# Kernel tuning notes

Measured on AMD Instinct MI355X. Metric: run time of the kernel, lower is better.

The kernel has to match this reference:

```python
import jax, jax.numpy as jnp
import numpy as np

EPSILON = 0.1
ALPHA = 0.5
N_ITER = 10
N_USERS = 100000


def setup_inputs() -> dict:
    key = jax.random.key(0)
    k1, k2, k3, k4, k5, k6 = jax.random.split(key, 6)
    B, C, F = 2048, 1024, 128
    users = jax.random.randint(k1, (B,), 0, N_USERS)
    items = jax.random.randint(k2, (B, C), 0, C)
    D = jax.random.uniform(k3, (B, C), minval=0.1, maxval=1.0)
    capacities = jax.random.uniform(k4, (C,), minval=0.5, maxval=1.5)
    # ScaledEmbedding: normal init scaled down by embedding_dim
    item_emb = jax.random.normal(k5, (C, F), dtype=jnp.float32) / F
    user_emb = jax.random.normal(k6, (N_USERS, F), dtype=jnp.float32) / F
    return dict(users=users, items=items, D=D, capacities=capacities,
                item_emb=item_emb, user_emb=user_emb)


def reference(users, items, D, capacities, item_emb, user_emb):
    B, C = D.shape
    ie = item_emb[items]            # [B, C, F] gathered candidate embeddings
    ue = user_emb[users]            # [B, F]
    dot = jnp.einsum('bcf,bf->bc', ie, ue)          # batched dot products
    affinity = (1.0 - ALPHA) * dot - ALPHA * (D / jnp.mean(D))
    K = jnp.exp(affinity / EPSILON)                 # [B, C]

    scaling = B / N_USERS
    a = jnp.ones((B,), K.dtype)
    b = capacities * scaling                        # [C]

    def step(carry, _):
        _, v = carry
        u = a / (K @ v)                             # [B]
        v_new = b / (K.T @ u)                       # [C]
        return (u, v_new), None

    (u, v), _ = jax.lax.scan(step, (a, jnp.ones((C,), K.dtype)),
                             None, length=N_ITER)
    P = K * (u[:, None] * v[None, :])               # K * outer(u, v)
    return P
```

## Files before the change

### kernel.cpp

```cpp
#include <hip/hip_runtime.h>
#include <hip/hip_fp16.h>

#define BB      2048
#define CC      1024
#define FF      128
#define NBLK    256
#define RPB     8
#define TPB     512
#define NITER   10
#define SUBR    8
#define SCALING_F (2048.0f / 100000.0f)

__device__ __align__(16) float g_K[BB * CC];
__device__ float g_meanPart[NBLK];
__device__ float g_colsum[NITER * SUBR * CC];

__global__ void __launch_bounds__(TPB)
k0_prep(const float* __restrict__ D) {
    const int bid = blockIdx.x, tid = threadIdx.x;
    for (int i = bid * TPB + tid; i < NITER * SUBR * CC; i += NBLK * TPB)
        g_colsum[i] = 0.0f;
    const float4* D4 = (const float4*)D;
    float p = 0.0f;
    for (int i = bid * TPB + tid; i < BB * CC / 4; i += NBLK * TPB) {
        float4 d = D4[i];
        p += d.x + d.y + d.z + d.w;
    }
    #pragma unroll
    for (int off = 32; off > 0; off >>= 1) p += __shfl_down(p, off, 64);
    __shared__ float red[TPB / 64];
    if ((tid & 63) == 0) red[tid >> 6] = p;
    __syncthreads();
    if (tid == 0) {
        float s = 0.0f;
        #pragma unroll
        for (int k = 0; k < TPB / 64; ++k) s += red[k];
        g_meanPart[bid] = s;
    }
}

__global__ void __launch_bounds__(TPB)
k1_buildK(const int* __restrict__ users, const int* __restrict__ items,
          const float* __restrict__ D, const float* __restrict__ iemb,
          const float* __restrict__ uemb) {
    const int bid = blockIdx.x, tid = threadIdx.x;
    const int r0 = bid * RPB;

    __shared__ float  uesh[RPB][FF];
    __shared__ __half dott[RPB][CC];
    __shared__ float  s2sh;

    if (tid < 256) {
        int r = tid >> 5, f4 = tid & 31;
        int u = users[r0 + r];
        ((float4*)uesh[r])[f4] = ((const float4*)(uemb + (size_t)u * FF))[f4];
    }
    if (tid < 64) {
        float s = g_meanPart[tid] + g_meanPart[tid + 64] +
                  g_meanPart[tid + 128] + g_meanPart[tid + 192];
        #pragma unroll
        for (int off = 32; off > 0; off >>= 1) s += __shfl_down(s, off, 64);
        if (tid == 0) s2sh = 5.0f * (float)(BB * CC) / s;
    }
    __syncthreads();

    const float4* us = (const float4*)uesh;
    #pragma unroll
    for (int jj = 0; jj < CC / TPB; ++jj) {
        int j = jj * TPB + tid;
        float acc[RPB] = {};
        const float4* ip = (const float4*)(iemb + (size_t)j * FF);
        for (int f4 = 0; f4 < FF / 4; ++f4) {
            float4 a = ip[f4];
            #pragma unroll
            for (int r = 0; r < RPB; ++r) {
                float4 b = us[r * (FF / 4) + f4];
                acc[r] += a.x * b.x + a.y * b.y + a.z * b.z + a.w * b.w;
            }
        }
        #pragma unroll
        for (int r = 0; r < RPB; ++r) dott[r][j] = __float2half(acc[r]);
    }
    __syncthreads();

    const float s2 = s2sh;
    const int4*   it4 = (const int4*)(items + ((size_t)r0 << 10));
    const float4* D4  = (const float4*)(D + ((size_t)r0 << 10));
    float4*       K4  = (float4*)(g_K + ((size_t)r0 << 10));
    for (int i = tid; i < RPB * CC / 4; i += TPB) {
        int4 iv = it4[i];
        float4 d = D4[i];
        int r = i >> 8;
        float4 kv;
        kv.x = __expf(5.0f * __half2float(dott[r][iv.x]) - s2 * d.x);
        kv.y = __expf(5.0f * __half2float(dott[r][iv.y]) - s2 * d.y);
        kv.z = __expf(5.0f * __half2float(dott[r][iv.z]) - s2 * d.z);
        kv.w = __expf(5.0f * __half2float(dott[r][iv.w]) - s2 * d.w);
        K4[i] = kv;
    }
}

__global__ void __launch_bounds__(TPB)
k_iter(const float* __restrict__ caps, int t) {
    const int bid = blockIdx.x, tid = threadIdx.x;
    const int r0 = bid * RPB;
    const int w = tid >> 6, l = tid & 63;

    __shared__ float Kt[RPB][CC];
    __shared__ float vsh[CC];
    __shared__ float ush[RPB];

    const float4* kr = (const float4*)(g_K + ((size_t)(r0 + w) << 10));
    float4 k4[4];
    #pragma unroll
    for (int j = 0; j < 4; ++j) k4[j] = kr[l + 64 * j];

    for (int c = tid; c < CC; c += TPB) {
        float v = 1.0f;
        if (t > 0) {
            const float* base = g_colsum + (size_t)(t - 1) * SUBR * CC;
            float s = 0.0f;
            #pragma unroll
            for (int k = 0; k < SUBR; ++k) s += base[k * CC + c];
            v = caps[c] * SCALING_F / s;
        }
        vsh[c] = v;
    }
    __syncthreads();

    {
        const float4* v4 = (const float4*)vsh;
        float4* KtF4 = (float4*)Kt[w];
        float p = 0.0f;
        #pragma unroll
        for (int j = 0; j < 4; ++j) {
            float4 v = v4[l + 64 * j];
            p += k4[j].x * v.x + k4[j].y * v.y + k4[j].z * v.z + k4[j].w * v.w;
            KtF4[l + 64 * j] = k4[j];
        }
        #pragma unroll
        for (int off = 32; off > 0; off >>= 1) p += __shfl_xor(p, off, 64);
        if (l == 0) ush[w] = 1.0f / p;
    }
    __syncthreads();

    {
        float sx = 0.0f, sy = 0.0f;
        #pragma unroll
        for (int r = 0; r < RPB; ++r) {
            float2 k = *(const float2*)&Kt[r][2 * tid];
            float ur = ush[r];
            sx += k.x * ur; sy += k.y * ur;
        }
        float* cb = g_colsum + ((size_t)t * SUBR + (bid & (SUBR - 1))) * CC
                  + 2 * tid;
        atomicAdd(cb, sx);
        atomicAdd(cb + 1, sy);
    }
}

__global__ void __launch_bounds__(TPB)
k_final(const float* __restrict__ caps, float* __restrict__ out) {
    const int bid = blockIdx.x, tid = threadIdx.x;
    const int r0 = bid * RPB;
    const int w = tid >> 6, l = tid & 63;

    __shared__ float vsh[CC];

    const float4* kr = (const float4*)(g_K + ((size_t)(r0 + w) << 10));
    float4 k4[4];
    #pragma unroll
    for (int j = 0; j < 4; ++j) k4[j] = kr[l + 64 * j];

    for (int c = tid; c < CC; c += TPB) {
        const float* base = g_colsum + (size_t)(NITER - 2) * SUBR * CC;
        float s = 0.0f;
        #pragma unroll
        for (int k = 0; k < SUBR; ++k) s += base[k * CC + c];
        vsh[c] = caps[c] * SCALING_F / s;
    }
    __syncthreads();

    float u;
    {
        const float4* v4 = (const float4*)vsh;
        float p = 0.0f;
        #pragma unroll
        for (int j = 0; j < 4; ++j) {
            float4 v = v4[l + 64 * j];
            p += k4[j].x * v.x + k4[j].y * v.y + k4[j].z * v.z + k4[j].w * v.w;
        }
        #pragma unroll
        for (int off = 32; off > 0; off >>= 1) p += __shfl_xor(p, off, 64);
        u = 1.0f / p;
    }
    __syncthreads();

    for (int c = tid; c < CC; c += TPB) {
        const float* base = g_colsum + (size_t)(NITER - 1) * SUBR * CC;
        float s = 0.0f;
        #pragma unroll
        for (int k = 0; k < SUBR; ++k) s += base[k * CC + c];
        vsh[c] = caps[c] * SCALING_F / s;
    }
    __syncthreads();

    {
        const float4* v4 = (const float4*)vsh;
        float4* o4 = (float4*)(out + ((size_t)(r0 + w) << 10));
        #pragma unroll
        for (int j = 0; j < 4; ++j) {
            float4 v = v4[l + 64 * j];
            float4 p;
            p.x = k4[j].x * u * v.x;  p.y = k4[j].y * u * v.y;
            p.z = k4[j].z * u * v.z;  p.w = k4[j].w * u * v.w;
            o4[l + 64 * j] = p;
        }
    }
}

extern "C" void kernel_launch(void* const* d_in, const int* in_sizes, int n_in,
                              void* d_out, int out_size, void* d_ws, size_t ws_size,
                              hipStream_t stream) {
    const int*   users = (const int*)d_in[0];
    const int*   items = (const int*)d_in[1];
    const float* D     = (const float*)d_in[2];
    const float* caps  = (const float*)d_in[3];
    const float* iemb  = (const float*)d_in[4];
    const float* uemb  = (const float*)d_in[5];
    float* out = (float*)d_out;

    hipLaunchKernelGGL(k0_prep,   dim3(NBLK), dim3(TPB), 0, stream, D);
    hipLaunchKernelGGL(k1_buildK, dim3(NBLK), dim3(TPB), 0, stream,
                       users, items, D, iemb, uemb);
    for (int t = 0; t < NITER; ++t)
        hipLaunchKernelGGL(k_iter, dim3(NBLK), dim3(TPB), 0, stream, caps, t);
    hipLaunchKernelGGL(k_final,  dim3(NBLK), dim3(TPB), 0, stream, caps, out);
}
```

Baseline: 193.1 us.

## Fuse all Sinkhorn stages into one persistent cooperative kernel with grid barriers

Replaces the thirteen separate kernel launches with a single cooperative kernel. Blocks sync through a custom sense-reversing grid barrier on global atomics. Each block's K slab stays resident in LDS across all iterations instead of being written to and re-read from global memory, and the D mean is computed in the same pass that stages D into LDS. This is meant to remove launch overhead and global K traffic, at the cost of grid-wide barrier latency and a dependence on all 256 blocks being co-resident.

```diff
diff --git a/kernel.cpp b/kernel.cpp
--- a/kernel.cpp
+++ b/kernel.cpp
@@ -9,211 +9,207 @@
 #define TPB     512
 #define NITER   10
 #define SUBR    8
+#define KSTRIDE 1028
 #define SCALING_F (2048.0f / 100000.0f)
 
-__device__ __align__(16) float g_K[BB * CC];
+__device__ int   g_barCnt;
+__device__ int   g_barFlag;
 __device__ float g_meanPart[NBLK];
 __device__ float g_colsum[NITER * SUBR * CC];
 
+__device__ __forceinline__ void grid_bar() {
+    __syncthreads();
+    if (threadIdx.x == 0) {
+        int sense = __hip_atomic_load(&g_barFlag, __ATOMIC_RELAXED,
+                                      __HIP_MEMORY_SCOPE_AGENT);
+        asm volatile("s_waitcnt vmcnt(0)" ::: "memory");
+        int old = __hip_atomic_fetch_add(&g_barCnt, 1, __ATOMIC_RELAXED,
+                                         __HIP_MEMORY_SCOPE_AGENT);
+        if (old == NBLK - 1) {
+            __hip_atomic_store(&g_barCnt, 0, __ATOMIC_RELAXED,
+                               __HIP_MEMORY_SCOPE_AGENT);
+            asm volatile("s_waitcnt vmcnt(0)" ::: "memory");
+            __hip_atomic_store(&g_barFlag, sense ^ 1, __ATOMIC_RELAXED,
+                               __HIP_MEMORY_SCOPE_AGENT);
+        } else {
+            while (__hip_atomic_load(&g_barFlag, __ATOMIC_RELAXED,
+                                     __HIP_MEMORY_SCOPE_AGENT) == sense)
+                __builtin_amdgcn_s_sleep(1);
+        }
+    }
+    __syncthreads();
+}
+
+#define WAIT_MY_ATOMICS() asm volatile("s_waitcnt vmcnt(0)" ::: "memory")
+
 __global__ void __launch_bounds__(TPB)
-k0_prep(const float* __restrict__ D) {
-    const int bid = blockIdx.x, tid = threadIdx.x;
-    for (int i = bid * TPB + tid; i < NITER * SUBR * CC; i += NBLK * TPB)
-        g_colsum[i] = 0.0f;
-    const float4* D4 = (const float4*)D;
-    float p = 0.0f;
-    for (int i = bid * TPB + tid; i < BB * CC / 4; i += NBLK * TPB) {
-        float4 d = D4[i];
-        p += d.x + d.y + d.z + d.w;
-    }
-    #pragma unroll
-    for (int off = 32; off > 0; off >>= 1) p += __shfl_down(p, off, 64);
-    __shared__ float red[TPB / 64];
-    if ((tid & 63) == 0) red[tid >> 6] = p;
-    __syncthreads();
-    if (tid == 0) {
-        float s = 0.0f;
-        #pragma unroll
-        for (int k = 0; k < TPB / 64; ++k) s += red[k];
-        g_meanPart[bid] = s;
-    }
-}
-
-__global__ void __launch_bounds__(TPB)
-k1_buildK(const int* __restrict__ users, const int* __restrict__ items,
-          const float* __restrict__ D, const float* __restrict__ iemb,
-          const float* __restrict__ uemb) {
+sink_all(const int* __restrict__ users, const int* __restrict__ items,
+         const float* __restrict__ D, const float* __restrict__ caps,
+         const float* __restrict__ iemb, const float* __restrict__ uemb,
+         float* __restrict__ out)
+{
     const int bid = blockIdx.x, tid = threadIdx.x;
     const int r0 = bid * RPB;
-
-    __shared__ float  uesh[RPB][FF];
-    __shared__ __half dott[RPB][CC];
-    __shared__ float  s2sh;
-
+    const int w = tid >> 6, l = tid & 63;
+
+    __shared__ __align__(16) float  Kt[RPB][KSTRIDE];
+    __shared__ __align__(16) __half dott[RPB][CC];
+    __shared__ __align__(16) float  uesh[RPB][FF];
+    __shared__ __align__(16) float  vsh[CC];
+    __shared__ __align__(16) float  capsh[CC];
+    __shared__ float ush[RPB];
+    __shared__ float red[RPB];
+
+    if (tid < (NITER * SUBR * CC) / NBLK)
+        __hip_atomic_store(&g_colsum[bid * 320 + tid], 0.0f,
+                           __ATOMIC_RELAXED, __HIP_MEMORY_SCOPE_AGENT);
+
+    float psum = 0.0f;
+    {
+        const float4* D4 = (const float4*)(D + ((size_t)r0 << 10));
+        for (int i = tid; i < RPB * CC / 4; i += TPB) {
+            float4 d = D4[i];
+            int r = i >> 8, c4 = (i & 255) << 2;
+            *(float4*)&Kt[r][c4] = d;
+            psum += d.x + d.y + d.z + d.w;
+        }
+    }
     if (tid < 256) {
         int r = tid >> 5, f4 = tid & 31;
         int u = users[r0 + r];
         ((float4*)uesh[r])[f4] = ((const float4*)(uemb + (size_t)u * FF))[f4];
     }
-    if (tid < 64) {
-        float s = g_meanPart[tid] + g_meanPart[tid + 64] +
-                  g_meanPart[tid + 128] + g_meanPart[tid + 192];
-        #pragma unroll
-        for (int off = 32; off > 0; off >>= 1) s += __shfl_down(s, off, 64);
-        if (tid == 0) s2sh = 5.0f * (float)(BB * CC) / s;
-    }
-    __syncthreads();
-
-    const float4* us = (const float4*)uesh;
-    #pragma unroll
-    for (int jj = 0; jj < CC / TPB; ++jj) {
-        int j = jj * TPB + tid;
-        float acc[RPB] = {};
-        const float4* ip = (const float4*)(iemb + (size_t)j * FF);
+    for (int c = tid; c < CC; c += TPB) capsh[c] = caps[c] * SCALING_F;
+    {
+        float p = psum;
+        #pragma unroll
+        for (int off = 32; off > 0; off >>= 1) p += __shfl_xor(p, off, 64);
+        if (l == 0) red[w] = p;
+    }
+    __syncthreads();
+    if (tid == 0) {
+        float s = 0.0f;
+        #pragma unroll
+        for (int k = 0; k < RPB; ++k) s += red[k];
+        __hip_atomic_store(&g_meanPart[bid], s,
+                           __ATOMIC_RELAXED, __HIP_MEMORY_SCOPE_AGENT);
+    }
+
+    {
+        float acc0[RPB] = {}, acc1[RPB] = {};
+        const float4* ip0 = (const float4*)(iemb + (size_t)tid * FF);
+        const float4* ip1 = (const float4*)(iemb + (size_t)(tid + TPB) * FF);
         for (int f4 = 0; f4 < FF / 4; ++f4) {
-            float4 a = ip[f4];
+            float4 a0 = ip0[f4], a1 = ip1[f4];
             #pragma unroll
             for (int r = 0; r < RPB; ++r) {
-                float4 b = us[r * (FF / 4) + f4];
-                acc[r] += a.x * b.x + a.y * b.y + a.z * b.z + a.w * b.w;
-            }
-        }
-        #pragma unroll
-        for (int r = 0; r < RPB; ++r) dott[r][j] = __float2half(acc[r]);
-    }
-    __syncthreads();
-
-    const float s2 = s2sh;
-    const int4*   it4 = (const int4*)(items + ((size_t)r0 << 10));
-    const float4* D4  = (const float4*)(D + ((size_t)r0 << 10));
-    float4*       K4  = (float4*)(g_K + ((size_t)r0 << 10));
-    for (int i = tid; i < RPB * CC / 4; i += TPB) {
-        int4 iv = it4[i];
-        float4 d = D4[i];
-        int r = i >> 8;
-        float4 kv;
-        kv.x = __expf(5.0f * __half2float(dott[r][iv.x]) - s2 * d.x);
-        kv.y = __expf(5.0f * __half2float(dott[r][iv.y]) - s2 * d.y);
-        kv.z = __expf(5.0f * __half2float(dott[r][iv.z]) - s2 * d.z);
-        kv.w = __expf(5.0f * __half2float(dott[r][iv.w]) - s2 * d.w);
-        K4[i] = kv;
-    }
-}
-
-__global__ void __launch_bounds__(TPB)
-k_iter(const float* __restrict__ caps, int t) {
-    const int bid = blockIdx.x, tid = threadIdx.x;
-    const int r0 = bid * RPB;
-    const int w = tid >> 6, l = tid & 63;
-
-    __shared__ float Kt[RPB][CC];
-    __shared__ float vsh[CC];
-    __shared__ float ush[RPB];
-
-    const float4* kr = (const float4*)(g_K + ((size_t)(r0 + w) << 10));
-    float4 k4[4];
-    #pragma unroll
-    for (int j = 0; j < 4; ++j) k4[j] = kr[l + 64 * j];
-
-    for (int c = tid; c < CC; c += TPB) {
-        float v = 1.0f;
-        if (t > 0) {
+                float4 b = ((const float4*)uesh[r])[f4];
+                acc0[r] += a0.x * b.x + a0.y * b.y + a0.z * b.z + a0.w * b.w;
+                acc1[r] += a1.x * b.x + a1.y * b.y + a1.z * b.z + a1.w * b.w;
+            }
+        }
+        #pragma unroll
+        for (int r = 0; r < RPB; ++r) {
+            dott[r][tid]       = __float2half(acc0[r]);
+            dott[r][tid + TPB] = __float2half(acc1[r]);
+        }
+    }
+
+    WAIT_MY_ATOMICS();
+    grid_bar();
+
+    if (tid < 256) {
+        float v = __hip_atomic_load(&g_meanPart[tid], __ATOMIC_RELAXED,
+                                    __HIP_MEMORY_SCOPE_AGENT);
+        #pragma unroll
+        for (int off = 32; off > 0; off >>= 1) v += __shfl_xor(v, off, 64);
+        if (l == 0) red[w] = v;
+    }
+    __syncthreads();
+    const float s2 = 5.0f * (float)(BB * CC) / (red[0] + red[1] + red[2] + red[3]);
+    {
+        const int4* it4 = (const int4*)(items + ((size_t)r0 << 10));
+        for (int i = tid; i < RPB * CC / 4; i += TPB) {
+            int4 iv = it4[i];
+            int r = i >> 8, c4 = (i & 255) << 2;
+            float4 d = *(float4*)&Kt[r][c4];
+            float4 kv;
+            kv.x = __expf(5.0f * __half2float(dott[r][iv.x]) - s2 * d.x);
+            kv.y = __expf(5.0f * __half2float(dott[r][iv.y]) - s2 * d.y);
+            kv.z = __expf(5.0f * __half2float(dott[r][iv.z]) - s2 * d.z);
+            kv.w = __expf(5.0f * __half2float(dott[r][iv.w]) - s2 * d.w);
+            *(float4*)&Kt[r][c4] = kv;
+        }
+    }
+    __syncthreads();
+
+    for (int t = 0; t < NITER; ++t) {
+        if (t == 0) {
+            for (int c = tid; c < CC; c += TPB) vsh[c] = 1.0f;
+        } else {
             const float* base = g_colsum + (size_t)(t - 1) * SUBR * CC;
+            for (int c = tid; c < CC; c += TPB) {
+                float s = 0.0f;
+                #pragma unroll
+                for (int k = 0; k < SUBR; ++k)
+                    s += __hip_atomic_load(&base[k * CC + c], __ATOMIC_RELAXED,
+                                           __HIP_MEMORY_SCOPE_AGENT);
+                vsh[c] = capsh[c] / s;
+            }
+        }
+        __syncthreads();
+        {
+            const float4* kr = (const float4*)Kt[w];
+            const float4* v4 = (const float4*)vsh;
+            float p = 0.0f;
+            #pragma unroll
+            for (int j = 0; j < 4; ++j) {
+                float4 k = kr[l + 64 * j], v = v4[l + 64 * j];
+                p += k.x * v.x + k.y * v.y + k.z * v.z + k.w * v.w;
+            }
+            #pragma unroll
+            for (int off = 32; off > 0; off >>= 1) p += __shfl_xor(p, off, 64);
+            if (l == 0) ush[w] = 1.0f / p;
+        }
+        __syncthreads();
+        {
+            float sx = 0.0f, sy = 0.0f;
+            #pragma unroll
+            for (int r = 0; r < RPB; ++r) {
+                float2 k = *(const float2*)&Kt[r][2 * tid];
+                float ur = ush[r];
+                sx += k.x * ur; sy += k.y * ur;
+            }
+            float* cb = g_colsum + ((size_t)t * SUBR + (bid & (SUBR - 1))) * CC
+                      + 2 * tid;
+            atomicAdd(cb, sx);
+            atomicAdd(cb + 1, sy);
+        }
+        WAIT_MY_ATOMICS();
+        grid_bar();
+    }
+
+    {
+        const float* base = g_colsum + (size_t)(NITER - 1) * SUBR * CC;
+        for (int c = tid; c < CC; c += TPB) {
             float s = 0.0f;
             #pragma unroll
-            for (int k = 0; k < SUBR; ++k) s += base[k * CC + c];
-            v = caps[c] * SCALING_F / s;
-        }
-        vsh[c] = v;
-    }
-    __syncthreads();
-
-    {
+            for (int k = 0; k < SUBR; ++k)
+                s += __hip_atomic_load(&base[k * CC + c], __ATOMIC_RELAXED,
+                                       __HIP_MEMORY_SCOPE_AGENT);
+            vsh[c] = capsh[c] / s;
+        }
+        __syncthreads();
+        const float4* kr = (const float4*)Kt[w];
         const float4* v4 = (const float4*)vsh;
-        float4* KtF4 = (float4*)Kt[w];
-        float p = 0.0f;
+        const float u = ush[w];
+        float4* o4 = (float4*)(out + ((size_t)(r0 + w) << 10));
         #pragma unroll
         for (int j = 0; j < 4; ++j) {
-            float4 v = v4[l + 64 * j];
-            p += k4[j].x * v.x + k4[j].y * v.y + k4[j].z * v.z + k4[j].w * v.w;
-            KtF4[l + 64 * j] = k4[j];
-        }
-        #pragma unroll
-        for (int off = 32; off > 0; off >>= 1) p += __shfl_xor(p, off, 64);
-        if (l == 0) ush[w] = 1.0f / p;
-    }
-    __syncthreads();
-
-    {
-        float sx = 0.0f, sy = 0.0f;
-        #pragma unroll
-        for (int r = 0; r < RPB; ++r) {
-            float2 k = *(const float2*)&Kt[r][2 * tid];
-            float ur = ush[r];
-            sx += k.x * ur; sy += k.y * ur;
-        }
-        float* cb = g_colsum + ((size_t)t * SUBR + (bid & (SUBR - 1))) * CC
-                  + 2 * tid;
-        atomicAdd(cb, sx);
-        atomicAdd(cb + 1, sy);
-    }
-}
-
-__global__ void __launch_bounds__(TPB)
-k_final(const float* __restrict__ caps, float* __restrict__ out) {
-    const int bid = blockIdx.x, tid = threadIdx.x;
-    const int r0 = bid * RPB;
-    const int w = tid >> 6, l = tid & 63;
-
-    __shared__ float vsh[CC];
-
-    const float4* kr = (const float4*)(g_K + ((size_t)(r0 + w) << 10));
-    float4 k4[4];
-    #pragma unroll
-    for (int j = 0; j < 4; ++j) k4[j] = kr[l + 64 * j];
-
-    for (int c = tid; c < CC; c += TPB) {
-        const float* base = g_colsum + (size_t)(NITER - 2) * SUBR * CC;
-        float s = 0.0f;
-        #pragma unroll
-        for (int k = 0; k < SUBR; ++k) s += base[k * CC + c];
-        vsh[c] = caps[c] * SCALING_F / s;
-    }
-    __syncthreads();
-
-    float u;
-    {
-        const float4* v4 = (const float4*)vsh;
-        float p = 0.0f;
-        #pragma unroll
-        for (int j = 0; j < 4; ++j) {
-            float4 v = v4[l + 64 * j];
-            p += k4[j].x * v.x + k4[j].y * v.y + k4[j].z * v.z + k4[j].w * v.w;
-        }
-        #pragma unroll
-        for (int off = 32; off > 0; off >>= 1) p += __shfl_xor(p, off, 64);
-        u = 1.0f / p;
-    }
-    __syncthreads();
-
-    for (int c = tid; c < CC; c += TPB) {
-        const float* base = g_colsum + (size_t)(NITER - 1) * SUBR * CC;
-        float s = 0.0f;
-        #pragma unroll
-        for (int k = 0; k < SUBR; ++k) s += base[k * CC + c];
-        vsh[c] = caps[c] * SCALING_F / s;
-    }
-    __syncthreads();
-
-    {
-        const float4* v4 = (const float4*)vsh;
-        float4* o4 = (float4*)(out + ((size_t)(r0 + w) << 10));
-        #pragma unroll
-        for (int j = 0; j < 4; ++j) {
-            float4 v = v4[l + 64 * j];
+            float4 k = kr[l + 64 * j], v = v4[l + 64 * j];
             float4 p;
-            p.x = k4[j].x * u * v.x;  p.y = k4[j].y * u * v.y;
-            p.z = k4[j].z * u * v.z;  p.w = k4[j].w * u * v.w;
+            p.x = k.x * u * v.x;  p.y = k.y * u * v.y;
+            p.z = k.z * u * v.z;  p.w = k.w * u * v.w;
             o4[l + 64 * j] = p;
         }
     }
@@ -230,10 +226,8 @@
     const float* uemb  = (const float*)d_in[5];
     float* out = (float*)d_out;
 
-    hipLaunchKernelGGL(k0_prep,   dim3(NBLK), dim3(TPB), 0, stream, D);
-    hipLaunchKernelGGL(k1_buildK, dim3(NBLK), dim3(TPB), 0, stream,
-                       users, items, D, iemb, uemb);
-    for (int t = 0; t < NITER; ++t)
-        hipLaunchKernelGGL(k_iter, dim3(NBLK), dim3(TPB), 0, stream, caps, t);
-    hipLaunchKernelGGL(k_final,  dim3(NBLK), dim3(TPB), 0, stream, caps, out);
+    void* args[] = { (void*)&users, (void*)&items, (void*)&D, (void*)&caps,
+                     (void*)&iemb, (void*)&uemb, (void*)&out };
+    hipLaunchCooperativeKernel((void*)sink_all, dim3(NBLK), dim3(TPB),
+                               args, 0, stream);
 }
```

New measurement: 302.2 us. 1.57x slower.

## Fuse prep into buildK with grid-wide spin barrier; reuse final u

Applied to the files above, without the earlier changes.

Removes the separate prep kernel. D-mean partials and colsum zeroing now happen inside buildK, and a monotonic counter acts as a grid-wide barrier so the dot-product work overlaps the wait. D is staged in shared memory so it is read from global memory only once. The last iteration stores u to global memory, so the final kernel no longer recomputes u from the previous colsum. The spin barrier needs all 256 blocks to be co-resident, and the larger shared footprint may lower occupancy.

```diff
diff --git a/kernel.cpp b/kernel.cpp
--- a/kernel.cpp
+++ b/kernel.cpp
@@ -9,35 +9,15 @@
 #define TPB     512
 #define NITER   10
 #define SUBR    8
+#define LINE    32
+#define CSLICE  ((NITER * SUBR * CC) / NBLK)
 #define SCALING_F (2048.0f / 100000.0f)
 
-__device__ __align__(16) float g_K[BB * CC];
-__device__ float g_meanPart[NBLK];
+__device__ int   g_cnt[8 * LINE];
+__device__ float g_meanPart[NBLK * LINE];
+__device__ float g_K[BB * CC];
 __device__ float g_colsum[NITER * SUBR * CC];
-
-__global__ void __launch_bounds__(TPB)
-k0_prep(const float* __restrict__ D) {
-    const int bid = blockIdx.x, tid = threadIdx.x;
-    for (int i = bid * TPB + tid; i < NITER * SUBR * CC; i += NBLK * TPB)
-        g_colsum[i] = 0.0f;
-    const float4* D4 = (const float4*)D;
-    float p = 0.0f;
-    for (int i = bid * TPB + tid; i < BB * CC / 4; i += NBLK * TPB) {
-        float4 d = D4[i];
-        p += d.x + d.y + d.z + d.w;
-    }
-    #pragma unroll
-    for (int off = 32; off > 0; off >>= 1) p += __shfl_down(p, off, 64);
-    __shared__ float red[TPB / 64];
-    if ((tid & 63) == 0) red[tid >> 6] = p;
-    __syncthreads();
-    if (tid == 0) {
-        float s = 0.0f;
-        #pragma unroll
-        for (int k = 0; k < TPB / 64; ++k) s += red[k];
-        g_meanPart[bid] = s;
-    }
-}
+__device__ float g_u[BB];
 
 __global__ void __launch_bounds__(TPB)
 k1_buildK(const int* __restrict__ users, const int* __restrict__ items,
@@ -45,52 +25,103 @@
           const float* __restrict__ uemb) {
     const int bid = blockIdx.x, tid = threadIdx.x;
     const int r0 = bid * RPB;
-
-    __shared__ float  uesh[RPB][FF];
-    __shared__ __half dott[RPB][CC];
-    __shared__ float  s2sh;
-
+    const int w = tid >> 6, l = tid & 63;
+
+    __shared__ __align__(16) float  Dsh[RPB][CC];
+    __shared__ __align__(16) __half dott[RPB][CC];
+    __shared__ __align__(16) float  uesh[RPB][FF];
+    __shared__ float red[RPB];
+    __shared__ float s2sh;
+
+    int target = 0;
+    if (w == 0) {
+        int c = (l < 8) ? __hip_atomic_load(&g_cnt[l * LINE], __ATOMIC_RELAXED,
+                                            __HIP_MEMORY_SCOPE_AGENT) : 0;
+        #pragma unroll
+        for (int off = 32; off > 0; off >>= 1) c += __shfl_xor(c, off, 64);
+        target = (c / NBLK + 1) * NBLK;
+    }
+
+    if (tid < CSLICE) g_colsum[bid * CSLICE + tid] = 0.0f;
+
+    float psum = 0.0f;
+    {
+        const float4* D4 = (const float4*)(D + ((size_t)r0 << 10));
+        for (int i = tid; i < RPB * CC / 4; i += TPB) {
+            float4 d = D4[i];
+            int r = i >> 8, c4 = (i & 255) << 2;
+            *(float4*)&Dsh[r][c4] = d;
+            psum += d.x + d.y + d.z + d.w;
+        }
+        #pragma unroll
+        for (int off = 32; off > 0; off >>= 1) psum += __shfl_xor(psum, off, 64);
+        if (l == 0) red[w] = psum;
+    }
     if (tid < 256) {
         int r = tid >> 5, f4 = tid & 31;
         int u = users[r0 + r];
         ((float4*)uesh[r])[f4] = ((const float4*)(uemb + (size_t)u * FF))[f4];
     }
-    if (tid < 64) {
-        float s = g_meanPart[tid] + g_meanPart[tid + 64] +
-                  g_meanPart[tid + 128] + g_meanPart[tid + 192];
-        #pragma unroll
-        for (int off = 32; off > 0; off >>= 1) s += __shfl_down(s, off, 64);
-        if (tid == 0) s2sh = 5.0f * (float)(BB * CC) / s;
-    }
-    __syncthreads();
-
-    const float4* us = (const float4*)uesh;
-    #pragma unroll
-    for (int jj = 0; jj < CC / TPB; ++jj) {
-        int j = jj * TPB + tid;
-        float acc[RPB] = {};
-        const float4* ip = (const float4*)(iemb + (size_t)j * FF);
+    __syncthreads();
+    if (tid == 0) {
+        float s = 0.0f;
+        #pragma unroll
+        for (int k = 0; k < RPB; ++k) s += red[k];
+        __hip_atomic_store(&g_meanPart[bid * LINE], s,
+                           __ATOMIC_RELAXED, __HIP_MEMORY_SCOPE_AGENT);
+        asm volatile("s_waitcnt vmcnt(0)" ::: "memory");
+        __hip_atomic_fetch_add(&g_cnt[(bid & 7) * LINE], 1,
+                               __ATOMIC_RELAXED, __HIP_MEMORY_SCOPE_AGENT);
+    }
+
+    {
+        float acc0[RPB] = {}, acc1[RPB] = {};
+        const float4* ip0 = (const float4*)(iemb + (size_t)tid * FF);
+        const float4* ip1 = (const float4*)(iemb + (size_t)(tid + TPB) * FF);
         for (int f4 = 0; f4 < FF / 4; ++f4) {
-            float4 a = ip[f4];
+            float4 a0 = ip0[f4], a1 = ip1[f4];
             #pragma unroll
             for (int r = 0; r < RPB; ++r) {
-                float4 b = us[r * (FF / 4) + f4];
-                acc[r] += a.x * b.x + a.y * b.y + a.z * b.z + a.w * b.w;
+                float4 b = ((const float4*)uesh[r])[f4];
+                acc0[r] += a0.x * b.x + a0.y * b.y + a0.z * b.z + a0.w * b.w;
+                acc1[r] += a1.x * b.x + a1.y * b.y + a1.z * b.z + a1.w * b.w;
             }
         }
         #pragma unroll
-        for (int r = 0; r < RPB; ++r) dott[r][j] = __float2half(acc[r]);
+        for (int r = 0; r < RPB; ++r) {
+            dott[r][tid]       = __float2half(acc0[r]);
+            dott[r][tid + TPB] = __float2half(acc1[r]);
+        }
+    }
+    __syncthreads();
+
+    if (w == 0) {
+        for (;;) {
+            int c = (l < 8) ? __hip_atomic_load(&g_cnt[l * LINE], __ATOMIC_RELAXED,
+                                                __HIP_MEMORY_SCOPE_AGENT) : 0;
+            #pragma unroll
+            for (int off = 32; off > 0; off >>= 1) c += __shfl_xor(c, off, 64);
+            if (c >= target) break;
+            __builtin_amdgcn_s_sleep(4);
+        }
+        float m = 0.0f;
+        #pragma unroll
+        for (int k = 0; k < 4; ++k)
+            m += __hip_atomic_load(&g_meanPart[(l + 64 * k) * LINE],
+                                   __ATOMIC_RELAXED, __HIP_MEMORY_SCOPE_AGENT);
+        #pragma unroll
+        for (int off = 32; off > 0; off >>= 1) m += __shfl_xor(m, off, 64);
+        if (l == 0) s2sh = 5.0f * (float)(BB * CC) / m;
     }
     __syncthreads();
 
     const float s2 = s2sh;
-    const int4*   it4 = (const int4*)(items + ((size_t)r0 << 10));
-    const float4* D4  = (const float4*)(D + ((size_t)r0 << 10));
-    float4*       K4  = (float4*)(g_K + ((size_t)r0 << 10));
+    const int4* it4 = (const int4*)(items + ((size_t)r0 << 10));
+    float4*     K4  = (float4*)(g_K + ((size_t)r0 << 10));
     for (int i = tid; i < RPB * CC / 4; i += TPB) {
         int4 iv = it4[i];
-        float4 d = D4[i];
-        int r = i >> 8;
+        int r = i >> 8, c4 = (i & 255) << 2;
+        float4 d = *(float4*)&Dsh[r][c4];
         float4 kv;
         kv.x = __expf(5.0f * __half2float(dott[r][iv.x]) - s2 * d.x);
         kv.y = __expf(5.0f * __half2float(dott[r][iv.y]) - s2 * d.y);
@@ -106,8 +137,8 @@
     const int r0 = bid * RPB;
     const int w = tid >> 6, l = tid & 63;
 
-    __shared__ float Kt[RPB][CC];
-    __shared__ float vsh[CC];
+    __shared__ __align__(16) float Kt[RPB][CC];
+    __shared__ __align__(16) float vsh[CC];
     __shared__ float ush[RPB];
 
     const float4* kr = (const float4*)(g_K + ((size_t)(r0 + w) << 10));
@@ -140,7 +171,11 @@
         }
         #pragma unroll
         for (int off = 32; off > 0; off >>= 1) p += __shfl_xor(p, off, 64);
-        if (l == 0) ush[w] = 1.0f / p;
+        if (l == 0) {
+            float u = 1.0f / p;
+            ush[w] = u;
+            if (t == NITER - 1) g_u[r0 + w] = u;
+        }
     }
     __syncthreads();
 
@@ -165,43 +200,22 @@
     const int r0 = bid * RPB;
     const int w = tid >> 6, l = tid & 63;
 
-    __shared__ float vsh[CC];
-
+    __shared__ __align__(16) float vsh[CC];
+
+    const float u = g_u[r0 + w];
     const float4* kr = (const float4*)(g_K + ((size_t)(r0 + w) << 10));
     float4 k4[4];
     #pragma unroll
     for (int j = 0; j < 4; ++j) k4[j] = kr[l + 64 * j];
 
-    for (int c = tid; c < CC; c += TPB) {
-        const float* base = g_colsum + (size_t)(NITER - 2) * SUBR * CC;
-        float s = 0.0f;
-        #pragma unroll
-        for (int k = 0; k < SUBR; ++k) s += base[k * CC + c];
-        vsh[c] = caps[c] * SCALING_F / s;
-    }
-    __syncthreads();
-
-    float u;
-    {
-        const float4* v4 = (const float4*)vsh;
-        float p = 0.0f;
-        #pragma unroll
-        for (int j = 0; j < 4; ++j) {
-            float4 v = v4[l + 64 * j];
-            p += k4[j].x * v.x + k4[j].y * v.y + k4[j].z * v.z + k4[j].w * v.w;
-        }
-        #pragma unroll
-        for (int off = 32; off > 0; off >>= 1) p += __shfl_xor(p, off, 64);
-        u = 1.0f / p;
-    }
-    __syncthreads();
-
-    for (int c = tid; c < CC; c += TPB) {
+    {
         const float* base = g_colsum + (size_t)(NITER - 1) * SUBR * CC;
-        float s = 0.0f;
-        #pragma unroll
-        for (int k = 0; k < SUBR; ++k) s += base[k * CC + c];
-        vsh[c] = caps[c] * SCALING_F / s;
+        for (int c = tid; c < CC; c += TPB) {
+            float s = 0.0f;
+            #pragma unroll
+            for (int k = 0; k < SUBR; ++k) s += base[k * CC + c];
+            vsh[c] = caps[c] * SCALING_F / s;
+        }
     }
     __syncthreads();
 
@@ -230,10 +244,9 @@
     const float* uemb  = (const float*)d_in[5];
     float* out = (float*)d_out;
 
-    hipLaunchKernelGGL(k0_prep,   dim3(NBLK), dim3(TPB), 0, stream, D);
     hipLaunchKernelGGL(k1_buildK, dim3(NBLK), dim3(TPB), 0, stream,
                        users, items, D, iemb, uemb);
     for (int t = 0; t < NITER; ++t)
         hipLaunchKernelGGL(k_iter, dim3(NBLK), dim3(TPB), 0, stream, caps, t);
-    hipLaunchKernelGGL(k_final,  dim3(NBLK), dim3(TPB), 0, stream, caps, out);
-}
+    hipLaunchKernelGGL(k_final, dim3(NBLK), dim3(TPB), 0, stream, caps, out);
+}
```

Measured after the change: 207.6 us. 7.6% more time.
